# Performance work log

Hardware: AMD Instinct MI355X
Metric: run time of the kernel (lower is better)

Reference implementation:

```python
import jax, jax.numpy as jnp
import numpy as np

OUT_H, OUT_W = 7, 7          # pooled output size
SR = 2                        # sampling_ratio (samples per bin side)
SCALE = 0.25                  # spatial_scale (stride-4 FPN level)
EPS = 1e-8


def setup_inputs() -> dict:
    key = jax.random.key(0)
    k1, k2, k3, k4, k5, k6 = jax.random.split(key, 6)
    N, C, H, W = 2, 256, 200, 200
    R = 1000
    inp = jax.random.normal(k1, (N, C, H, W), dtype=jnp.float32)
    # rois: (batch_idx, x_ctr, y_ctr, width, height, angle_degrees) in image coords
    bidx = jax.random.randint(k2, (R,), 0, N).astype(jnp.float32)
    xc = jax.random.uniform(k3, (R,), minval=0.0, maxval=W / SCALE)
    yc = jax.random.uniform(k4, (R,), minval=0.0, maxval=H / SCALE)
    wh = jax.random.uniform(k5, (R, 2), minval=32.0, maxval=256.0)
    ang = jax.random.uniform(k6, (R,), minval=-90.0, maxval=90.0)
    rois = jnp.concatenate([bidx[:, None], xc[:, None], yc[:, None], wh, ang[:, None]], axis=1)
    return {"input": inp, "rois": rois}


def _roi_align_rotated(feat, rois):
    """Detectron2-style rotated RoIAlign (aligned, continuous coords).
    feat: [N,C,H,W] float; rois: [R,6] -> out [R,C,OUT_H,OUT_W]."""
    N, C, H, W = feat.shape
    R = rois.shape[0]
    b = rois[:, 0].astype(jnp.int32)
    cw = rois[:, 1] * SCALE - 0.5          # roi center (continuous pixel coords)
    ch = rois[:, 2] * SCALE - 0.5
    rw = jnp.maximum(rois[:, 3] * SCALE, 1.0)
    rh = jnp.maximum(rois[:, 4] * SCALE, 1.0)
    theta = rois[:, 5] * jnp.float32(np.pi / 180.0)
    cos_t, sin_t = jnp.cos(theta), jnp.sin(theta)

    bin_h = rh / OUT_H
    bin_w = rw / OUT_W
    # sample offsets within each bin: (i + 0.5)/SR for i in [0, SR)
    frac = (jnp.arange(SR, dtype=feat.dtype) + 0.5) / SR
    # local (un-rotated) coords relative to roi center: [R, OUT, SR]
    yy = (-rh / 2)[:, None, None] + (jnp.arange(OUT_H, dtype=feat.dtype)[None, :, None] + frac[None, None, :]) * bin_h[:, None, None]
    xx = (-rw / 2)[:, None, None] + (jnp.arange(OUT_W, dtype=feat.dtype)[None, :, None] + frac[None, None, :]) * bin_w[:, None, None]
    # rotate into feature-map coords: [R, PH, PW, GH, GW]
    yy5 = yy[:, :, None, :, None]
    xx5 = xx[:, None, :, None, :]
    c5 = cos_t[:, None, None, None, None]
    s5 = sin_t[:, None, None, None, None]
    y = yy5 * c5 - xx5 * s5 + ch[:, None, None, None, None]
    x = yy5 * s5 + xx5 * c5 + cw[:, None, None, None, None]

    S = OUT_H * OUT_W * SR * SR
    y = y.reshape(R, S)
    x = x.reshape(R, S)

    valid = (y >= -1.0) & (y <= H) & (x >= -1.0) & (x <= W)
    y = jnp.maximum(y, 0.0)
    x = jnp.maximum(x, 0.0)
    yl0 = jnp.floor(y).astype(jnp.int32)
    xl0 = jnp.floor(x).astype(jnp.int32)
    cy = yl0 >= H - 1
    cx = xl0 >= W - 1
    y_low = jnp.where(cy, H - 1, yl0)
    y_high = jnp.where(cy, H - 1, yl0 + 1)
    yv = jnp.where(cy, jnp.asarray(H - 1, feat.dtype), y)
    x_low = jnp.where(cx, W - 1, xl0)
    x_high = jnp.where(cx, W - 1, xl0 + 1)
    xv = jnp.where(cx, jnp.asarray(W - 1, feat.dtype), x)

    ly = yv - y_low.astype(feat.dtype)
    lx = xv - x_low.astype(feat.dtype)
    hy, hx = 1.0 - ly, 1.0 - lx
    w1, w2, w3, w4 = hy * hx, hy * lx, ly * hx, ly * lx

    bb = b[:, None]  # [R,1] broadcast against [R,S]
    v1 = feat[bb, :, y_low, x_low]    # [R,S,C]
    v2 = feat[bb, :, y_low, x_high]
    v3 = feat[bb, :, y_high, x_low]
    v4 = feat[bb, :, y_high, x_high]
    val = (w1[..., None] * v1 + w2[..., None] * v2
           + w3[..., None] * v3 + w4[..., None] * v4)
    val = jnp.where(valid[..., None], val, 0.0)
    # average over the SR*SR samples in each bin
    out = val.reshape(R, OUT_H, OUT_W, SR * SR, C).sum(axis=3) / (SR * SR)
    return out.transpose(0, 3, 1, 2)  # [R,C,PH,PW]


def reference(input, rois):
    out = _roi_align_rotated(input, rois)
    # wrapper applies torch.nan_to_num(roi_align, EPS, EPS, EPS)
    return jnp.nan_to_num(out, nan=EPS, posinf=EPS, neginf=EPS)
```

## Files before the change

### kernel.cpp

```cpp
#include <hip/hip_runtime.h>
#include <hip/hip_fp16.h>

#define FH 200
#define FW 200
#define FHW 40000
#define FC 256
#define NBIN 49
#define NSAMP 196
#define OHS 66

typedef float  nfloat4 __attribute__((ext_vector_type(4)));

__device__ __forceinline__ void compute_sample(const float* __restrict__ roi,
                                               int s, bool nhwc,
                                               float4* wout, int4* oout)
{
    int   b  = (int)roi[0];
    float cw = roi[1] * 0.25f - 0.5f;
    float ch = roi[2] * 0.25f - 0.5f;
    float rw = fmaxf(roi[3] * 0.25f, 1.0f);
    float rh = fmaxf(roi[4] * 0.25f, 1.0f);
    float th = roi[5] * 0.017453292519943295f;
    float ct = __cosf(th);
    float st = __sinf(th);
    float bin_h = rh / 7.0f;
    float bin_w = rw / 7.0f;

    int bin = s >> 2;
    int sub = s & 3;
    int iy  = sub >> 1;
    int ix  = sub & 1;
    int ph  = bin / 7;
    int pw  = bin - ph * 7;

    float fy = 0.25f + 0.5f * (float)iy;
    float fx = 0.25f + 0.5f * (float)ix;
    float yy = -rh * 0.5f + ((float)ph + fy) * bin_h;
    float xx = -rw * 0.5f + ((float)pw + fx) * bin_w;
    float y  = yy * ct - xx * st + ch;
    float x  = yy * st + xx * ct + cw;

    bool valid = (y >= -1.0f) && (y <= (float)FH) && (x >= -1.0f) && (x <= (float)FW);
    y = fmaxf(y, 0.0f);
    x = fmaxf(x, 0.0f);
    int y0 = (int)floorf(y);
    int x0 = (int)floorf(x);
    bool cy = (y0 >= FH - 1);
    bool cx = (x0 >= FW - 1);
    int ylo = cy ? (FH - 1) : y0;
    int yhi = cy ? (FH - 1) : (y0 + 1);
    int xlo = cx ? (FW - 1) : x0;
    int xhi = cx ? (FW - 1) : (x0 + 1);
    float ly = cy ? 0.0f : (y - (float)y0);
    float lx = cx ? 0.0f : (x - (float)x0);
    float hy = 1.0f - ly;
    float hx = 1.0f - lx;
    float m  = valid ? 0.25f : 0.0f;

    *wout = make_float4(hy * hx * m, hy * lx * m, ly * hx * m, ly * lx * m);

    int bb = b * (FC * FHW);
    int p0 = ylo * FW + xlo;
    int p1 = ylo * FW + xhi;
    int p2 = yhi * FW + xlo;
    int p3 = yhi * FW + xhi;
    if (nhwc)
        *oout = make_int4(bb + p0 * FC, bb + p1 * FC, bb + p2 * FC, bb + p3 * FC);
    else
        *oout = make_int4(bb + p0, bb + p1, bb + p2, bb + p3);
}

__device__ __forceinline__ float fixnum(float v)
{
    return (v == v && v <= 3.402823466e38f && v >= -3.402823466e38f) ? v : 1e-8f;
}

__global__ __launch_bounds__(256)
void transpose_f16_kernel(const float* __restrict__ in, __half* __restrict__ out)
{
    __shared__ __align__(16) __half tileT[32][72];
    int b   = blockIdx.z;
    int p0  = blockIdx.x * 32;
    int c0  = blockIdx.y * 64;
    int tid = threadIdx.x;

    const float* inb  = in  + (size_t)b * FC * FHW;
    __half*      outb = out + (size_t)b * FHW * FC;

#pragma unroll
    for (int k = 0; k < 2; ++k) {
        int chl = k * 32 + (tid >> 3);
        int px4 = (tid & 7) * 4;
        const nfloat4* src =
            (const nfloat4*)(inb + (size_t)(c0 + chl) * FHW + p0 + px4);
        nfloat4 v = __builtin_nontemporal_load(src);
        int g   = ((chl >> 3) ^ (px4 >> 2)) & 7;
        int col = (g << 3) | (chl & 7);
        tileT[px4 + 0][col] = __float2half(v.x);
        tileT[px4 + 1][col] = __float2half(v.y);
        tileT[px4 + 2][col] = __float2half(v.z);
        tileT[px4 + 3][col] = __float2half(v.w);
    }
    __syncthreads();

    int p = tid >> 3;
    int q = tid & 7;
    int g = (q ^ ((p >> 2) & 7));
    uint4 d = *(const uint4*)&tileT[p][g << 3];
    *(uint4*)(outb + (size_t)(p0 + p) * FC + c0 + q * 8) = d;
}

__global__ __launch_bounds__(512, 4)
void roi_nhwc_f16_kernel(const __half* __restrict__ feat,
                         const float* __restrict__ rois,
                         float* __restrict__ out)
{
    __shared__ __align__(16) uint4 s_wh[NSAMP];
    __shared__ __align__(16) int4  s_o[NSAMP];
    __shared__ __half out_h[NBIN * OHS];

    int bid = blockIdx.x;
    int q   = (bid >> 1) & 3;
    int r   = (bid >> 3) * 2 + (bid & 1);
    int c0  = q * 64;
    int tid = threadIdx.x;

    const float* roi = rois + r * 6;
    if (tid < NSAMP) {
        float4 w; int4 o;
        compute_sample(roi, tid, true, &w, &o);
        __half2 wh[4];
        wh[0] = __half2half2(__float2half(w.x));
        wh[1] = __half2half2(__float2half(w.y));
        wh[2] = __half2half2(__float2half(w.z));
        wh[3] = __half2half2(__float2half(w.w));
        s_wh[tid] = *(const uint4*)wh;
        s_o[tid]  = o;
    }
    __syncthreads();

    int grp   = tid >> 3;
    int lane8 = tid & 7;
    int ch8   = lane8 * 8;

    if (grp < NBIN) {
        const __half* fbase = feat + c0 + ch8;

        uint4 la[16];
#pragma unroll
        for (int sub = 0; sub < 4; ++sub) {
            int4 o = s_o[grp * 4 + sub];
            la[sub * 4 + 0] = *(const uint4*)(fbase + o.x);
            la[sub * 4 + 1] = *(const uint4*)(fbase + o.y);
            la[sub * 4 + 2] = *(const uint4*)(fbase + o.z);
            la[sub * 4 + 3] = *(const uint4*)(fbase + o.w);
        }

        __half2 acc[4];
#pragma unroll
        for (int j = 0; j < 4; ++j) acc[j] = __half2half2(__float2half(0.0f));
#pragma unroll
        for (int sub = 0; sub < 4; ++sub) {
            uint4 whu = s_wh[grp * 4 + sub];
            const __half2* wh = (const __half2*)&whu;
#pragma unroll
            for (int c = 0; c < 4; ++c) {
                const __half2* h = (const __half2*)&la[sub * 4 + c];
#pragma unroll
                for (int j = 0; j < 4; ++j)
                    acc[j] = __hfma2(wh[c], h[j], acc[j]);
            }
        }
        __half2* dst = (__half2*)&out_h[grp * OHS + ch8];
#pragma unroll
        for (int j = 0; j < 4; ++j) dst[j] = acc[j];
    }
    __syncthreads();

    float* obase = out + (size_t)r * (FC * NBIN) + (size_t)c0 * NBIN;
    for (int v4 = tid; v4 < (64 * NBIN) / 4; v4 += 512) {
        int f0 = v4 * 4;
        nfloat4 vals;
#pragma unroll
        for (int i = 0; i < 4; ++i) {
            int f = f0 + i;
            int c = f / NBIN;
            int b = f - c * NBIN;
            vals[i] = fixnum(__half2float(out_h[b * OHS + c]));
        }
        __builtin_nontemporal_store(vals, (nfloat4*)(obase + f0));
    }
}

__global__ __launch_bounds__(256)
void roi_nchw_kernel(const float* __restrict__ feat,
                     const float* __restrict__ rois,
                     float* __restrict__ out)
{
    int r   = blockIdx.x;
    int tid = threadIdx.x;

    __shared__ float4 s_w[NSAMP];
    __shared__ int4   s_o[NSAMP];

    const float* roi = rois + r * 6;
    if (tid < NSAMP) {
        float4 w; int4 o;
        compute_sample(roi, tid, false, &w, &o);
        s_w[tid] = w;
        s_o[tid] = o;
    }
    __syncthreads();

    const float* fc = feat + (size_t)tid * FHW;
    float* obase = out + (size_t)r * (FC * NBIN) + (size_t)tid * NBIN;

    for (int bin = 0; bin < NBIN; ++bin) {
        float a = 0.0f;
#pragma unroll
        for (int k = 0; k < 4; ++k) {
            float4 w = s_w[bin * 4 + k];
            int4   o = s_o[bin * 4 + k];
            a += w.x * fc[o.x] + w.y * fc[o.y] + w.z * fc[o.z] + w.w * fc[o.w];
        }
        obase[bin] = fixnum(a);
    }
}

extern "C" void kernel_launch(void* const* d_in, const int* in_sizes, int n_in,
                              void* d_out, int out_size, void* d_ws, size_t ws_size,
                              hipStream_t stream)
{
    const float* feat = (const float*)d_in[0];
    const float* rois = (const float*)d_in[1];
    float* out = (float*)d_out;

    int R = in_sizes[1] / 6;
    int N = in_sizes[0] / (FC * FHW);
    size_t need = (size_t)in_sizes[0] * sizeof(__half);

    if (ws_size >= need) {
        __half* featT = (__half*)d_ws;
        dim3 tg(FHW / 32, FC / 64, N);
        transpose_f16_kernel<<<tg, 256, 0, stream>>>(feat, featT);
        roi_nhwc_f16_kernel<<<dim3(R * 4, 1, 1), 512, 0, stream>>>(featT, rois, out);
    } else {
        roi_nchw_kernel<<<R, 256, 0, stream>>>(feat, rois, out);
    }
}
```

Baseline: 165.3 us.

## Process RoIs in Morton order of their centers to improve cache locality

Adds a single-block bitonic sort kernel that orders RoIs by a Morton (Z-order) code of their quantized centers. The main RoI kernel reads through this permutation, so blocks that run at the same time gather from nearby feature-map regions and hit shared L2/MALL. It costs an extra kernel launch with a serial 1024-element sort, and the key ignores batch index, so spatially close RoIs from different images still land together.

```diff
diff --git a/kernel.cpp b/kernel.cpp
--- a/kernel.cpp
+++ b/kernel.cpp
@@ -75,6 +75,46 @@
     return (v == v && v <= 3.402823466e38f && v >= -3.402823466e38f) ? v : 1e-8f;
 }
 
+__global__ __launch_bounds__(1024)
+void sort_rois_kernel(const float* __restrict__ rois, int R,
+                      int* __restrict__ perm)
+{
+    int t = threadIdx.x;
+    if (R > 1024) {
+        for (int i = t; i < R; i += 1024) perm[i] = i;
+        return;
+    }
+    __shared__ unsigned int keys[1024];
+    unsigned int key = 0xFFFFFFFFu;
+    if (t < R) {
+        float cx = rois[t * 6 + 1] * 0.25f;
+        float cy = rois[t * 6 + 2] * 0.25f;
+        int qx = min(255, max(0, (int)(cx * 1.28f)));
+        int qy = min(255, max(0, (int)(cy * 1.28f)));
+        unsigned int m = 0;
+#pragma unroll
+        for (int i = 0; i < 8; ++i)
+            m |= (((qx >> i) & 1u) << (2 * i)) | (((qy >> i) & 1u) << (2 * i + 1));
+        key = (m << 12) | (unsigned int)t;
+    }
+    keys[t] = key;
+    __syncthreads();
+#pragma unroll 1
+    for (int k = 2; k <= 1024; k <<= 1) {
+#pragma unroll 1
+        for (int j = k >> 1; j > 0; j >>= 1) {
+            int ixj = t ^ j;
+            if (ixj > t) {
+                unsigned int a = keys[t], b = keys[ixj];
+                bool up = ((t & k) == 0);
+                if ((a > b) == up) { keys[t] = b; keys[ixj] = a; }
+            }
+            __syncthreads();
+        }
+    }
+    if (t < R) perm[t] = (int)(keys[t] & 0xFFFu);
+}
+
 __global__ __launch_bounds__(256)
 void transpose_f16_kernel(const float* __restrict__ in, __half* __restrict__ out)
 {
@@ -113,6 +153,7 @@
 __global__ __launch_bounds__(512, 4)
 void roi_nhwc_f16_kernel(const __half* __restrict__ feat,
                          const float* __restrict__ rois,
+                         const int* __restrict__ perm,
                          float* __restrict__ out)
 {
     __shared__ __align__(16) uint4 s_wh[NSAMP];
@@ -122,10 +163,11 @@
     int bid = blockIdx.x;
     int q   = (bid >> 1) & 3;
     int r   = (bid >> 3) * 2 + (bid & 1);
+    int rs  = perm[r];
     int c0  = q * 64;
     int tid = threadIdx.x;
 
-    const float* roi = rois + r * 6;
+    const float* roi = rois + rs * 6;
     if (tid < NSAMP) {
         float4 w; int4 o;
         compute_sample(roi, tid, true, &w, &o);
@@ -177,7 +219,7 @@
     }
     __syncthreads();
 
-    float* obase = out + (size_t)r * (FC * NBIN) + (size_t)c0 * NBIN;
+    float* obase = out + (size_t)rs * (FC * NBIN) + (size_t)c0 * NBIN;
     for (int v4 = tid; v4 < (64 * NBIN) / 4; v4 += 512) {
         int f0 = v4 * 4;
         nfloat4 vals;
@@ -237,13 +279,16 @@
 
     int R = in_sizes[1] / 6;
     int N = in_sizes[0] / (FC * FHW);
-    size_t need = (size_t)in_sizes[0] * sizeof(__half);
-
-    if (ws_size >= need) {
+    size_t featT_halves = (size_t)N * FC * FHW;
+    size_t need = featT_halves * sizeof(__half) + (size_t)R * sizeof(int);
+
+    if (ws_size >= need && (R & 1) == 0) {
         __half* featT = (__half*)d_ws;
+        int*    perm  = (int*)((char*)d_ws + featT_halves * sizeof(__half));
+        sort_rois_kernel<<<1, 1024, 0, stream>>>(rois, R, perm);
         dim3 tg(FHW / 32, FC / 64, N);
         transpose_f16_kernel<<<tg, 256, 0, stream>>>(feat, featT);
-        roi_nhwc_f16_kernel<<<dim3(R * 4, 1, 1), 512, 0, stream>>>(featT, rois, out);
+        roi_nhwc_f16_kernel<<<dim3(R * 4, 1, 1), 512, 0, stream>>>(featT, rois, perm, out);
     } else {
         roi_nchw_kernel<<<R, 256, 0, stream>>>(feat, rois, out);
     }
```

Measured after the change: 166.7 us. Within noise of the previous version (+0.9%).
